# Performance work log

Measured on AMD Instinct MI355X. Metric: run time of the kernel, lower is better.

Reference implementation:

```python
import jax, jax.numpy as jnp
import numpy as np

N_G, K = 1024, 64
n_G, k = 32, 8          # n_G = sqrt(N_G), k = sqrt(K)
m = n_G * k             # 256
M = N_G * K             # 65536

def _mask_indices(k):
    # concentric square rings of a k x k grid; ring 0 = outermost
    ii, jj = np.meshgrid(np.arange(k), np.arange(k), indexing='ij')
    d = np.minimum(np.minimum(ii, jj), np.minimum(k - 1 - ii, k - 1 - jj))
    rings = [(d == r) for r in range((k + 1) // 2)]
    groups = np.array_split(np.arange(len(rings)), 3)  # outer / inter / inner ring groups
    merged = [np.any(np.stack([rings[i] for i in g]), axis=0) for g in groups]
    outer, inter, inner = merged
    flat = lambda msk: np.nonzero(msk.ravel())[0]
    return flat(inner), flat(inter), flat(outer)

IDX_INNER, IDX_INTER, IDX_OUTER = _mask_indices(k)  # sizes 4, 12, 48

def setup_inputs() -> dict:
    key = jax.random.key(0)
    ks = jax.random.split(key, 13)
    p = lambda kk, sh: 0.05 * jax.random.normal(kk, sh, dtype=jnp.float32)
    return {
        'pgi': jax.random.normal(ks[0], (32, M, 3), dtype=jnp.float32),
        'W_lift': p(ks[1], (3, 32)),   'b_lift': p(ks[2], (32,)),
        'W_code': p(ks[3], (96, 128)), 'b_code': p(ks[4], (128,)),
        'W_h1': p(ks[5], (128, 64)),   'b_h1': p(ks[6], (64,)),
        'W_h2': p(ks[7], (64, 32)),    'b_h2': p(ks[8], (32,)),
        'W_h3': p(ks[9], (32, 16)),    'b_h3': p(ks[10], (16,)),
        'W_h4': p(ks[11], (16, 3)),    'b_h4': jnp.zeros((3,), jnp.float32),
    }

def _lift_max(pts, W, b):
    # pts: [B, N_G, n_sel, 3] -> SMLP(3->32, leakyrelu 0.2) -> max over points
    h = jax.nn.leaky_relu(jnp.einsum('bgpc,cd->bgpd', pts, W) + b, 0.2)
    return h.max(axis=2)  # [B, N_G, 32]

def reference(pgi, W_lift, b_lift, W_code, b_code, W_h1, b_h1, W_h2, b_h2, W_h3, b_h3, W_h4, b_h4):
    B = pgi.shape[0]
    # pgi [B, M, 3] is a row-major m x m grid; partition into N_G blocks of k x k points
    grid = pgi.reshape(B, n_G, k, n_G, k, 3)
    blocks = grid.transpose(0, 1, 3, 2, 4, 5).reshape(B, N_G, K, 3)
    v_inner = _lift_max(blocks[:, :, IDX_INNER], W_lift, b_lift)
    v_inter = _lift_max(blocks[:, :, IDX_INTER], W_lift, b_lift)
    v_outer = _lift_max(blocks[:, :, IDX_OUTER], W_lift, b_lift)
    v = jnp.concatenate([v_inner, v_inter, v_outer], axis=-1)   # [B, N_G, 96]
    v_code = jax.nn.leaky_relu(v @ W_code + b_code, 0.2)        # [B, N_G, 128]
    h = jax.nn.relu(v_code @ W_h1 + b_h1)
    h = jax.nn.relu(h @ W_h2 + b_h2)
    h = jax.nn.relu(h @ W_h3 + b_h3)
    return h @ W_h4 + b_h4                                      # guidance_pts [B, N_G, 3]
```

## Files before the change

kernel.cpp:

```cpp
#include <hip/hip_runtime.h>
#include <math.h>


typedef _Float16 h8  __attribute__((ext_vector_type(8)));
typedef _Float16 h2t __attribute__((ext_vector_type(2)));
typedef float    f4  __attribute__((ext_vector_type(4)));

constexpr int SVH = 104;
constexpr int SWC = 104;
constexpr int SCH = 136;
constexpr int S1H = 72;
constexpr int S2H = 40;
constexpr int S3H = 24;

constexpr int OFF_V = 0;
constexpr int OFF_W = 13312;
constexpr int OFF_C = 39936;
constexpr int W1T_O = 0;
constexpr int W2T_O = 8704;
constexpr int W3T_O = 11008;

__global__ __launch_bounds__(256, 2)
void flatnet_fused(const float* __restrict__ pgi,
                   const float* __restrict__ Wl, const float* __restrict__ bl,
                   const float* __restrict__ Wc, const float* __restrict__ bc,
                   const float* __restrict__ W1, const float* __restrict__ b1,
                   const float* __restrict__ W2, const float* __restrict__ b2,
                   const float* __restrict__ W3, const float* __restrict__ b3,
                   const float* __restrict__ W4, const float* __restrict__ b4,
                   float* __restrict__ out)
{
    __shared__ __align__(16) char lds[57344];
    _Float16* sV = (_Float16*)(lds + OFF_V);
    _Float16* sW = (_Float16*)(lds + OFF_W);
    _Float16* sC = (_Float16*)(lds + OFF_C);

    const int t    = threadIdx.x;
    const int blk  = blockIdx.x;
    const int lane = t & 63;
    const int wv   = t >> 6;
    const int l15  = lane & 15;
    const int lq   = lane >> 4;

    {
        const int ln = t >> 2;
        const int q  = t & 3;
        const int gn = blk * 64 + ln;
        const int b  = gn >> 10;
        const int g  = gn & 1023;
        const int gi = g >> 5, gj = g & 31;

        float w0[8], w1[8], w2[8], bb[8];
        #pragma unroll
        for (int d = 0; d < 8; ++d) {
            const int dd = q * 8 + d;
            w0[d] = Wl[dd];
            w1[d] = Wl[32 + dd];
            w2[d] = Wl[64 + dd];
            bb[d] = bl[dd];
        }

        float gm[3][8];
        #pragma unroll
        for (int gg = 0; gg < 3; ++gg)
            #pragma unroll
            for (int d = 0; d < 8; ++d) gm[gg][d] = -INFINITY;

        constexpr int GT[8][8] = {
            {2,2,2,2,2,2,2,2},
            {2,2,2,2,2,2,2,2},
            {2,2,1,1,1,1,2,2},
            {2,2,1,0,0,1,2,2},
            {2,2,1,0,0,1,2,2},
            {2,2,1,1,1,1,2,2},
            {2,2,2,2,2,2,2,2},
            {2,2,2,2,2,2,2,2},
        };

        const size_t rowbase = (size_t)b * 65536 + ((size_t)gi * 8) * 256 + (size_t)gj * 8;
        #pragma unroll
        for (int pi = 0; pi < 8; ++pi) {
            const float4* src = (const float4*)(pgi + (rowbase + (size_t)pi * 256) * 3);
            float f[24];
            #pragma unroll
            for (int l = 0; l < 6; ++l) {
                const float4 v = src[l];
                f[l*4+0] = v.x; f[l*4+1] = v.y; f[l*4+2] = v.z; f[l*4+3] = v.w;
            }
            #pragma unroll
            for (int pj = 0; pj < 8; ++pj) {
                const int grp = GT[pi][pj];
                const float x = f[pj*3], y = f[pj*3+1], z = f[pj*3+2];
                #pragma unroll
                for (int d = 0; d < 8; ++d) {
                    float v = fmaf(x, w0[d], bb[d]);
                    v = fmaf(y, w1[d], v);
                    v = fmaf(z, w2[d], v);
                    gm[grp][d] = fmaxf(gm[grp][d], v);
                }
            }
        }
        #pragma unroll
        for (int gg = 0; gg < 3; ++gg) {
            h8 hv;
            #pragma unroll
            for (int d = 0; d < 8; ++d) {
                const float v = gm[gg][d];
                hv[d] = (_Float16)fmaxf(v, 0.2f * v);
            }
            *(h8*)&sV[ln*SVH + gg*32 + q*8] = hv;
        }

        #pragma unroll
        for (int i = 0; i < 6; ++i) {
            const int u = t + (i << 8);
            const int k = (u >> 5) << 1;
            const int n = (u & 31) << 2;
            const float4 r0 = *(const float4*)&Wc[k*128 + n];
            const float4 r1 = *(const float4*)&Wc[(k+1)*128 + n];
            h2t p0 = {(_Float16)r0.x, (_Float16)r1.x};
            h2t p1 = {(_Float16)r0.y, (_Float16)r1.y};
            h2t p2 = {(_Float16)r0.z, (_Float16)r1.z};
            h2t p3 = {(_Float16)r0.w, (_Float16)r1.w};
            *(h2t*)&sW[(n+0)*SWC + k] = p0;
            *(h2t*)&sW[(n+1)*SWC + k] = p1;
            *(h2t*)&sW[(n+2)*SWC + k] = p2;
            *(h2t*)&sW[(n+3)*SWC + k] = p3;
        }
    }
    __syncthreads();

    {
        const int nt0 = wv * 2;
        h8 Bf[2][3];
        float bcv[2];
        #pragma unroll
        for (int nn = 0; nn < 2; ++nn) {
            bcv[nn] = bc[(nt0+nn)*16 + l15];
            #pragma unroll
            for (int kq = 0; kq < 3; ++kq)
                Bf[nn][kq] = *(const h8*)&sW[((nt0+nn)*16 + l15)*SWC + kq*32 + lq*8];
        }
        f4 acc[4][2];
        #pragma unroll
        for (int mt = 0; mt < 4; ++mt)
            #pragma unroll
            for (int nn = 0; nn < 2; ++nn) {
                f4 z = {bcv[nn], bcv[nn], bcv[nn], bcv[nn]};
                acc[mt][nn] = z;
            }
        #pragma unroll
        for (int mt = 0; mt < 4; ++mt) {
            h8 Af[3];
            #pragma unroll
            for (int kq = 0; kq < 3; ++kq)
                Af[kq] = *(const h8*)&sV[(mt*16 + l15)*SVH + kq*32 + lq*8];
            #pragma unroll
            for (int kq = 0; kq < 3; ++kq) {
                acc[mt][0] = __builtin_amdgcn_mfma_f32_16x16x32_f16(Af[kq], Bf[0][kq], acc[mt][0], 0, 0, 0);
                acc[mt][1] = __builtin_amdgcn_mfma_f32_16x16x32_f16(Af[kq], Bf[1][kq], acc[mt][1], 0, 0, 0);
            }
        }
        __syncthreads();

        #pragma unroll
        for (int mt = 0; mt < 4; ++mt)
            #pragma unroll
            for (int nn = 0; nn < 2; ++nn) {
                const int col = (nt0+nn)*16 + l15;
                #pragma unroll
                for (int r = 0; r < 4; ++r) {
                    const int row = mt*16 + lq*4 + r;
                    const float v = acc[mt][nn][r];
                    sC[row*SCH + col] = (_Float16)fmaxf(v, 0.2f * v);
                }
            }
    }

    {
        #pragma unroll
        for (int i = 0; i < 4; ++i) {
            const int u = t + (i << 8);
            const int k = (u >> 4) << 1;
            const int n = (u & 15) << 2;
            const float4 r0 = *(const float4*)&W1[k*64 + n];
            const float4 r1 = *(const float4*)&W1[(k+1)*64 + n];
            h2t p0 = {(_Float16)r0.x, (_Float16)r1.x};
            h2t p1 = {(_Float16)r0.y, (_Float16)r1.y};
            h2t p2 = {(_Float16)r0.z, (_Float16)r1.z};
            h2t p3 = {(_Float16)r0.w, (_Float16)r1.w};
            *(h2t*)&sW[W1T_O + (n+0)*SCH + k] = p0;
            *(h2t*)&sW[W1T_O + (n+1)*SCH + k] = p1;
            *(h2t*)&sW[W1T_O + (n+2)*SCH + k] = p2;
            *(h2t*)&sW[W1T_O + (n+3)*SCH + k] = p3;
        }
        {
            const int k = (t >> 3) << 1;
            const int n = (t & 7) << 2;
            const float4 r0 = *(const float4*)&W2[k*32 + n];
            const float4 r1 = *(const float4*)&W2[(k+1)*32 + n];
            h2t p0 = {(_Float16)r0.x, (_Float16)r1.x};
            h2t p1 = {(_Float16)r0.y, (_Float16)r1.y};
            h2t p2 = {(_Float16)r0.z, (_Float16)r1.z};
            h2t p3 = {(_Float16)r0.w, (_Float16)r1.w};
            *(h2t*)&sW[W2T_O + (n+0)*S1H + k] = p0;
            *(h2t*)&sW[W2T_O + (n+1)*S1H + k] = p1;
            *(h2t*)&sW[W2T_O + (n+2)*S1H + k] = p2;
            *(h2t*)&sW[W2T_O + (n+3)*S1H + k] = p3;
        }
        if (t < 64) {
            const int k = (t >> 2) << 1;
            const int n = (t & 3) << 2;
            const float4 r0 = *(const float4*)&W3[k*16 + n];
            const float4 r1 = *(const float4*)&W3[(k+1)*16 + n];
            h2t p0 = {(_Float16)r0.x, (_Float16)r1.x};
            h2t p1 = {(_Float16)r0.y, (_Float16)r1.y};
            h2t p2 = {(_Float16)r0.z, (_Float16)r1.z};
            h2t p3 = {(_Float16)r0.w, (_Float16)r1.w};
            *(h2t*)&sW[W3T_O + (n+0)*S2H + k] = p0;
            *(h2t*)&sW[W3T_O + (n+1)*S2H + k] = p1;
            *(h2t*)&sW[W3T_O + (n+2)*S2H + k] = p2;
            *(h2t*)&sW[W3T_O + (n+3)*S2H + k] = p3;
        }
    }
    __syncthreads();

    {
        h8 Bf[4];
        #pragma unroll
        for (int kq = 0; kq < 4; ++kq)
            Bf[kq] = *(const h8*)&sW[W1T_O + (wv*16 + l15)*SCH + kq*32 + lq*8];
        const float bv = b1[wv*16 + l15];
        f4 acc[4];
        #pragma unroll
        for (int mt = 0; mt < 4; ++mt) { f4 z = {bv,bv,bv,bv}; acc[mt] = z; }
        #pragma unroll
        for (int mt = 0; mt < 4; ++mt) {
            #pragma unroll
            for (int kq = 0; kq < 4; ++kq) {
                const h8 Af = *(const h8*)&sC[(mt*16 + l15)*SCH + kq*32 + lq*8];
                acc[mt] = __builtin_amdgcn_mfma_f32_16x16x32_f16(Af, Bf[kq], acc[mt], 0, 0, 0);
            }
        }
        __syncthreads();
        #pragma unroll
        for (int mt = 0; mt < 4; ++mt) {
            const int col = wv*16 + l15;
            #pragma unroll
            for (int r = 0; r < 4; ++r) {
                const int row = mt*16 + lq*4 + r;
                sV[row*S1H + col] = (_Float16)fmaxf(acc[mt][r], 0.f);
            }
        }
    }
    __syncthreads();

    {
        const int nt  = wv & 1;
        const int mt0 = (wv >> 1) << 1;
        h8 Bf[2];
        #pragma unroll
        for (int kq = 0; kq < 2; ++kq)
            Bf[kq] = *(const h8*)&sW[W2T_O + (nt*16 + l15)*S1H + kq*32 + lq*8];
        const float bv = b2[nt*16 + l15];
        f4 acc[2];
        #pragma unroll
        for (int mi = 0; mi < 2; ++mi) { f4 z = {bv,bv,bv,bv}; acc[mi] = z; }
        #pragma unroll
        for (int mi = 0; mi < 2; ++mi) {
            #pragma unroll
            for (int kq = 0; kq < 2; ++kq) {
                const h8 Af = *(const h8*)&sV[((mt0+mi)*16 + l15)*S1H + kq*32 + lq*8];
                acc[mi] = __builtin_amdgcn_mfma_f32_16x16x32_f16(Af, Bf[kq], acc[mi], 0, 0, 0);
            }
        }
        __syncthreads();
        #pragma unroll
        for (int mi = 0; mi < 2; ++mi) {
            const int col = nt*16 + l15;
            #pragma unroll
            for (int r = 0; r < 4; ++r) {
                const int row = (mt0+mi)*16 + lq*4 + r;
                sC[row*S2H + col] = (_Float16)fmaxf(acc[mi][r], 0.f);
            }
        }
    }
    __syncthreads();

    {
        const h8 Bf = *(const h8*)&sW[W3T_O + l15*S2H + lq*8];
        const float bv = b3[l15];
        f4 acc = {bv,bv,bv,bv};
        const h8 Af = *(const h8*)&sC[(wv*16 + l15)*S2H + lq*8];
        acc = __builtin_amdgcn_mfma_f32_16x16x32_f16(Af, Bf, acc, 0, 0, 0);
        #pragma unroll
        for (int r = 0; r < 4; ++r) {
            const int row = wv*16 + lq*4 + r;
            sC[2560 + row*S3H + l15] = (_Float16)fmaxf(acc[r], 0.f);
        }
    }
    __syncthreads();

    if (t < 64) {
        const h8 h0 = *(const h8*)&sC[2560 + t*S3H];
        const h8 h1 = *(const h8*)&sC[2560 + t*S3H + 8];
        float a[16];
        #pragma unroll
        for (int j = 0; j < 8; ++j) { a[j] = (float)h0[j]; a[8+j] = (float)h1[j]; }
        float acc0 = b4[0], acc1 = b4[1], acc2 = b4[2];
        #pragma unroll
        for (int j = 0; j < 16; ++j) {
            acc0 = fmaf(a[j], W4[j*3+0], acc0);
            acc1 = fmaf(a[j], W4[j*3+1], acc1);
            acc2 = fmaf(a[j], W4[j*3+2], acc2);
        }
        const size_t gn = (size_t)blk * 64 + t;
        out[gn*3 + 0] = acc0;
        out[gn*3 + 1] = acc1;
        out[gn*3 + 2] = acc2;
    }
}

extern "C" void kernel_launch(void* const* d_in, const int* in_sizes, int n_in,
                              void* d_out, int out_size, void* d_ws, size_t ws_size,
                              hipStream_t stream)
{
    const float* pgi = (const float*)d_in[0];
    const float* Wl  = (const float*)d_in[1];
    const float* bl  = (const float*)d_in[2];
    const float* Wc  = (const float*)d_in[3];
    const float* bc  = (const float*)d_in[4];
    const float* W1  = (const float*)d_in[5];
    const float* b1  = (const float*)d_in[6];
    const float* W2  = (const float*)d_in[7];
    const float* b2  = (const float*)d_in[8];
    const float* W3  = (const float*)d_in[9];
    const float* b3  = (const float*)d_in[10];
    const float* W4  = (const float*)d_in[11];
    const float* b4  = (const float*)d_in[12];

    hipLaunchKernelGGL(flatnet_fused, dim3(512), dim3(256), 0, stream,
                       pgi, Wl, bl, Wc, bc, W1, b1, W2, b2, W3, b3, W4, b4,
                       (float*)d_out);
}
```

Measured before the change: 101.0 us.

## Pre-convert weights in separate kernel, halve groups per block, split rows across threads

```diff
diff --git a/kernel.cpp b/kernel.cpp
--- a/kernel.cpp
+++ b/kernel.cpp
@@ -2,38 +2,56 @@
 #include <math.h>
 
 
-typedef _Float16 h8  __attribute__((ext_vector_type(8)));
-typedef _Float16 h2t __attribute__((ext_vector_type(2)));
-typedef float    f4  __attribute__((ext_vector_type(4)));
+typedef _Float16 h8 __attribute__((ext_vector_type(8)));
+typedef float    f4 __attribute__((ext_vector_type(4)));
+
+constexpr int WCT_O = 0;
+constexpr int W1T_O = 12288;
+constexpr int W2T_O = 20480;
+constexpr int W3T_O = 22528;
+constexpr int WS_N  = 23040;
 
 constexpr int SVH = 104;
-constexpr int SWC = 104;
 constexpr int SCH = 136;
 constexpr int S1H = 72;
 constexpr int S2H = 40;
 constexpr int S3H = 24;
-
-constexpr int OFF_V = 0;
-constexpr int OFF_W = 13312;
-constexpr int OFF_C = 39936;
-constexpr int W1T_O = 0;
-constexpr int W2T_O = 8704;
-constexpr int W3T_O = 11008;
-
-__global__ __launch_bounds__(256, 2)
+constexpr int H3O = 32 * S2H;
+
+__global__ __launch_bounds__(256)
+void cvt_weights(const float* __restrict__ Wc, const float* __restrict__ W1,
+                 const float* __restrict__ W2, const float* __restrict__ W3,
+                 _Float16* __restrict__ ws16)
+{
+    const int i = blockIdx.x * 256 + threadIdx.x;
+    float v;
+    if (i < 12288) {
+        const int n = i / 96, k = i - n * 96;
+        v = Wc[k * 128 + n];
+    } else if (i < 20480) {
+        const int j = i - 12288, n = j >> 7, k = j & 127;
+        v = W1[k * 64 + n];
+    } else if (i < 22528) {
+        const int j = i - 20480, n = j >> 6, k = j & 63;
+        v = W2[k * 32 + n];
+    } else {
+        const int j = i - 22528, n = j >> 5, k = j & 31;
+        v = W3[k * 16 + n];
+    }
+    ws16[i] = (_Float16)v;
+}
+
+__global__ __launch_bounds__(256, 4)
 void flatnet_fused(const float* __restrict__ pgi,
                    const float* __restrict__ Wl, const float* __restrict__ bl,
-                   const float* __restrict__ Wc, const float* __restrict__ bc,
-                   const float* __restrict__ W1, const float* __restrict__ b1,
-                   const float* __restrict__ W2, const float* __restrict__ b2,
-                   const float* __restrict__ W3, const float* __restrict__ b3,
+                   const _Float16* __restrict__ ws16,
+                   const float* __restrict__ bc, const float* __restrict__ b1,
+                   const float* __restrict__ b2, const float* __restrict__ b3,
                    const float* __restrict__ W4, const float* __restrict__ b4,
                    float* __restrict__ out)
 {
-    __shared__ __align__(16) char lds[57344];
-    _Float16* sV = (_Float16*)(lds + OFF_V);
-    _Float16* sW = (_Float16*)(lds + OFF_W);
-    _Float16* sC = (_Float16*)(lds + OFF_C);
+    __shared__ __align__(16) _Float16 sV[32 * SVH];
+    __shared__ __align__(16) _Float16 sC[32 * SCH];
 
     const int t    = threadIdx.x;
     const int blk  = blockIdx.x;
@@ -43,9 +61,11 @@
     const int lq   = lane >> 4;
 
     {
-        const int ln = t >> 2;
-        const int q  = t & 3;
-        const int gn = blk * 64 + ln;
+        const int ln = t >> 3;
+        const int q  = t & 7;
+        const int dq = (q & 3) * 8;
+        const int h  = q >> 2;
+        const int gn = blk * 32 + ln;
         const int b  = gn >> 10;
         const int g  = gn & 1023;
         const int gi = g >> 5, gj = g & 31;
@@ -53,11 +73,10 @@
         float w0[8], w1[8], w2[8], bb[8];
         #pragma unroll
         for (int d = 0; d < 8; ++d) {
-            const int dd = q * 8 + d;
-            w0[d] = Wl[dd];
-            w1[d] = Wl[32 + dd];
-            w2[d] = Wl[64 + dd];
-            bb[d] = bl[dd];
+            w0[d] = Wl[dq + d];
+            w1[d] = Wl[32 + dq + d];
+            w2[d] = Wl[64 + dq + d];
+            bb[d] = bl[dq + d];
         }
 
         float gm[3][8];
@@ -66,21 +85,18 @@
             #pragma unroll
             for (int d = 0; d < 8; ++d) gm[gg][d] = -INFINITY;
 
-        constexpr int GT[8][8] = {
+        constexpr int GT4[4][8] = {
             {2,2,2,2,2,2,2,2},
             {2,2,2,2,2,2,2,2},
             {2,2,1,1,1,1,2,2},
             {2,2,1,0,0,1,2,2},
-            {2,2,1,0,0,1,2,2},
-            {2,2,1,1,1,1,2,2},
-            {2,2,2,2,2,2,2,2},
-            {2,2,2,2,2,2,2,2},
         };
 
         const size_t rowbase = (size_t)b * 65536 + ((size_t)gi * 8) * 256 + (size_t)gj * 8;
         #pragma unroll
-        for (int pi = 0; pi < 8; ++pi) {
-            const float4* src = (const float4*)(pgi + (rowbase + (size_t)pi * 256) * 3);
+        for (int pi = 0; pi < 4; ++pi) {
+            const int prow = h ? (7 - pi) : pi;
+            const float4* src = (const float4*)(pgi + (rowbase + (size_t)prow * 256) * 3);
             float f[24];
             #pragma unroll
             for (int l = 0; l < 6; ++l) {
@@ -89,7 +105,7 @@
             }
             #pragma unroll
             for (int pj = 0; pj < 8; ++pj) {
-                const int grp = GT[pi][pj];
+                const int grp = GT4[pi][pj];
                 const float x = f[pj*3], y = f[pj*3+1], z = f[pj*3+2];
                 #pragma unroll
                 for (int d = 0; d < 8; ++d) {
@@ -101,31 +117,22 @@
             }
         }
         #pragma unroll
-        for (int gg = 0; gg < 3; ++gg) {
-            h8 hv;
-            #pragma unroll
-            for (int d = 0; d < 8; ++d) {
-                const float v = gm[gg][d];
-                hv[d] = (_Float16)fmaxf(v, 0.2f * v);
-            }
-            *(h8*)&sV[ln*SVH + gg*32 + q*8] = hv;
-        }
-
-        #pragma unroll
-        for (int i = 0; i < 6; ++i) {
-            const int u = t + (i << 8);
-            const int k = (u >> 5) << 1;
-            const int n = (u & 31) << 2;
-            const float4 r0 = *(const float4*)&Wc[k*128 + n];
-            const float4 r1 = *(const float4*)&Wc[(k+1)*128 + n];
-            h2t p0 = {(_Float16)r0.x, (_Float16)r1.x};
-            h2t p1 = {(_Float16)r0.y, (_Float16)r1.y};
-            h2t p2 = {(_Float16)r0.z, (_Float16)r1.z};
-            h2t p3 = {(_Float16)r0.w, (_Float16)r1.w};
-            *(h2t*)&sW[(n+0)*SWC + k] = p0;
-            *(h2t*)&sW[(n+1)*SWC + k] = p1;
-            *(h2t*)&sW[(n+2)*SWC + k] = p2;
-            *(h2t*)&sW[(n+3)*SWC + k] = p3;
+        for (int gg = 0; gg < 3; ++gg)
+            #pragma unroll
+            for (int d = 0; d < 8; ++d)
+                gm[gg][d] = fmaxf(gm[gg][d], __shfl_xor(gm[gg][d], 4));
+
+        if (h == 0) {
+            #pragma unroll
+            for (int gg = 0; gg < 3; ++gg) {
+                h8 hv;
+                #pragma unroll
+                for (int d = 0; d < 8; ++d) {
+                    const float v = gm[gg][d];
+                    hv[d] = (_Float16)fmaxf(v, 0.2f * v);
+                }
+                *(h8*)&sV[ln*SVH + gg*32 + dq] = hv;
+            }
         }
     }
     __syncthreads();
@@ -139,32 +146,28 @@
             bcv[nn] = bc[(nt0+nn)*16 + l15];
             #pragma unroll
             for (int kq = 0; kq < 3; ++kq)
-                Bf[nn][kq] = *(const h8*)&sW[((nt0+nn)*16 + l15)*SWC + kq*32 + lq*8];
-        }
-        f4 acc[4][2];
-        #pragma unroll
-        for (int mt = 0; mt < 4; ++mt)
+                Bf[nn][kq] = *(const h8*)&ws16[WCT_O + ((nt0+nn)*16 + l15)*96 + kq*32 + lq*8];
+        }
+        f4 acc[2][2];
+        #pragma unroll
+        for (int mt = 0; mt < 2; ++mt)
             #pragma unroll
             for (int nn = 0; nn < 2; ++nn) {
                 f4 z = {bcv[nn], bcv[nn], bcv[nn], bcv[nn]};
                 acc[mt][nn] = z;
             }
         #pragma unroll
-        for (int mt = 0; mt < 4; ++mt) {
-            h8 Af[3];
-            #pragma unroll
-            for (int kq = 0; kq < 3; ++kq)
-                Af[kq] = *(const h8*)&sV[(mt*16 + l15)*SVH + kq*32 + lq*8];
+        for (int mt = 0; mt < 2; ++mt) {
             #pragma unroll
             for (int kq = 0; kq < 3; ++kq) {
-                acc[mt][0] = __builtin_amdgcn_mfma_f32_16x16x32_f16(Af[kq], Bf[0][kq], acc[mt][0], 0, 0, 0);
-                acc[mt][1] = __builtin_amdgcn_mfma_f32_16x16x32_f16(Af[kq], Bf[1][kq], acc[mt][1], 0, 0, 0);
+                const h8 Af = *(const h8*)&sV[(mt*16 + l15)*SVH + kq*32 + lq*8];
+                acc[mt][0] = __builtin_amdgcn_mfma_f32_16x16x32_f16(Af, Bf[0][kq], acc[mt][0], 0, 0, 0);
+                acc[mt][1] = __builtin_amdgcn_mfma_f32_16x16x32_f16(Af, Bf[1][kq], acc[mt][1], 0, 0, 0);
             }
         }
         __syncthreads();
-
-        #pragma unroll
-        for (int mt = 0; mt < 4; ++mt)
+        #pragma unroll
+        for (int mt = 0; mt < 2; ++mt)
             #pragma unroll
             for (int nn = 0; nn < 2; ++nn) {
                 const int col = (nt0+nn)*16 + l15;
@@ -176,75 +179,27 @@
                 }
             }
     }
-
-    {
-        #pragma unroll
-        for (int i = 0; i < 4; ++i) {
-            const int u = t + (i << 8);
-            const int k = (u >> 4) << 1;
-            const int n = (u & 15) << 2;
-            const float4 r0 = *(const float4*)&W1[k*64 + n];
-            const float4 r1 = *(const float4*)&W1[(k+1)*64 + n];
-            h2t p0 = {(_Float16)r0.x, (_Float16)r1.x};
-            h2t p1 = {(_Float16)r0.y, (_Float16)r1.y};
-            h2t p2 = {(_Float16)r0.z, (_Float16)r1.z};
-            h2t p3 = {(_Float16)r0.w, (_Float16)r1.w};
-            *(h2t*)&sW[W1T_O + (n+0)*SCH + k] = p0;
-            *(h2t*)&sW[W1T_O + (n+1)*SCH + k] = p1;
-            *(h2t*)&sW[W1T_O + (n+2)*SCH + k] = p2;
-            *(h2t*)&sW[W1T_O + (n+3)*SCH + k] = p3;
-        }
-        {
-            const int k = (t >> 3) << 1;
-            const int n = (t & 7) << 2;
-            const float4 r0 = *(const float4*)&W2[k*32 + n];
-            const float4 r1 = *(const float4*)&W2[(k+1)*32 + n];
-            h2t p0 = {(_Float16)r0.x, (_Float16)r1.x};
-            h2t p1 = {(_Float16)r0.y, (_Float16)r1.y};
-            h2t p2 = {(_Float16)r0.z, (_Float16)r1.z};
-            h2t p3 = {(_Float16)r0.w, (_Float16)r1.w};
-            *(h2t*)&sW[W2T_O + (n+0)*S1H + k] = p0;
-            *(h2t*)&sW[W2T_O + (n+1)*S1H + k] = p1;
-            *(h2t*)&sW[W2T_O + (n+2)*S1H + k] = p2;
-            *(h2t*)&sW[W2T_O + (n+3)*S1H + k] = p3;
-        }
-        if (t < 64) {
-            const int k = (t >> 2) << 1;
-            const int n = (t & 3) << 2;
-            const float4 r0 = *(const float4*)&W3[k*16 + n];
-            const float4 r1 = *(const float4*)&W3[(k+1)*16 + n];
-            h2t p0 = {(_Float16)r0.x, (_Float16)r1.x};
-            h2t p1 = {(_Float16)r0.y, (_Float16)r1.y};
-            h2t p2 = {(_Float16)r0.z, (_Float16)r1.z};
-            h2t p3 = {(_Float16)r0.w, (_Float16)r1.w};
-            *(h2t*)&sW[W3T_O + (n+0)*S2H + k] = p0;
-            *(h2t*)&sW[W3T_O + (n+1)*S2H + k] = p1;
-            *(h2t*)&sW[W3T_O + (n+2)*S2H + k] = p2;
-            *(h2t*)&sW[W3T_O + (n+3)*S2H + k] = p3;
-        }
-    }
     __syncthreads();
 
     {
         h8 Bf[4];
         #pragma unroll
         for (int kq = 0; kq < 4; ++kq)
-            Bf[kq] = *(const h8*)&sW[W1T_O + (wv*16 + l15)*SCH + kq*32 + lq*8];
+            Bf[kq] = *(const h8*)&ws16[W1T_O + (wv*16 + l15)*128 + kq*32 + lq*8];
         const float bv = b1[wv*16 + l15];
-        f4 acc[4];
-        #pragma unroll
-        for (int mt = 0; mt < 4; ++mt) { f4 z = {bv,bv,bv,bv}; acc[mt] = z; }
-        #pragma unroll
-        for (int mt = 0; mt < 4; ++mt) {
+        f4 acc[2];
+        #pragma unroll
+        for (int mt = 0; mt < 2; ++mt) { f4 z = {bv,bv,bv,bv}; acc[mt] = z; }
+        #pragma unroll
+        for (int mt = 0; mt < 2; ++mt)
             #pragma unroll
             for (int kq = 0; kq < 4; ++kq) {
                 const h8 Af = *(const h8*)&sC[(mt*16 + l15)*SCH + kq*32 + lq*8];
                 acc[mt] = __builtin_amdgcn_mfma_f32_16x16x32_f16(Af, Bf[kq], acc[mt], 0, 0, 0);
             }
-        }
         __syncthreads();
         #pragma unroll
-        for (int mt = 0; mt < 4; ++mt) {
+        for (int mt = 0; mt < 2; ++mt) {
             const int col = wv*16 + l15;
             #pragma unroll
             for (int r = 0; r < 4; ++r) {
@@ -256,54 +211,46 @@
     __syncthreads();
 
     {
-        const int nt  = wv & 1;
-        const int mt0 = (wv >> 1) << 1;
+        const int mt = wv & 1;
+        const int nt = wv >> 1;
         h8 Bf[2];
         #pragma unroll
         for (int kq = 0; kq < 2; ++kq)
-            Bf[kq] = *(const h8*)&sW[W2T_O + (nt*16 + l15)*S1H + kq*32 + lq*8];
+            Bf[kq] = *(const h8*)&ws16[W2T_O + (nt*16 + l15)*64 + kq*32 + lq*8];
         const float bv = b2[nt*16 + l15];
-        f4 acc[2];
-        #pragma unroll
-        for (int mi = 0; mi < 2; ++mi) { f4 z = {bv,bv,bv,bv}; acc[mi] = z; }
-        #pragma unroll
-        for (int mi = 0; mi < 2; ++mi) {
-            #pragma unroll
-            for (int kq = 0; kq < 2; ++kq) {
-                const h8 Af = *(const h8*)&sV[((mt0+mi)*16 + l15)*S1H + kq*32 + lq*8];
-                acc[mi] = __builtin_amdgcn_mfma_f32_16x16x32_f16(Af, Bf[kq], acc[mi], 0, 0, 0);
-            }
+        f4 acc = {bv, bv, bv, bv};
+        #pragma unroll
+        for (int kq = 0; kq < 2; ++kq) {
+            const h8 Af = *(const h8*)&sV[(mt*16 + l15)*S1H + kq*32 + lq*8];
+            acc = __builtin_amdgcn_mfma_f32_16x16x32_f16(Af, Bf[kq], acc, 0, 0, 0);
         }
         __syncthreads();
-        #pragma unroll
-        for (int mi = 0; mi < 2; ++mi) {
-            const int col = nt*16 + l15;
-            #pragma unroll
-            for (int r = 0; r < 4; ++r) {
-                const int row = (mt0+mi)*16 + lq*4 + r;
-                sC[row*S2H + col] = (_Float16)fmaxf(acc[mi][r], 0.f);
-            }
-        }
-    }
-    __syncthreads();
-
-    {
-        const h8 Bf = *(const h8*)&sW[W3T_O + l15*S2H + lq*8];
+        const int col = nt*16 + l15;
+        #pragma unroll
+        for (int r = 0; r < 4; ++r) {
+            const int row = mt*16 + lq*4 + r;
+            sC[row*S2H + col] = (_Float16)fmaxf(acc[r], 0.f);
+        }
+    }
+    __syncthreads();
+
+    if (wv < 2) {
+        const h8 Bf = *(const h8*)&ws16[W3T_O + l15*32 + lq*8];
         const float bv = b3[l15];
-        f4 acc = {bv,bv,bv,bv};
+        f4 acc = {bv, bv, bv, bv};
         const h8 Af = *(const h8*)&sC[(wv*16 + l15)*S2H + lq*8];
         acc = __builtin_amdgcn_mfma_f32_16x16x32_f16(Af, Bf, acc, 0, 0, 0);
         #pragma unroll
         for (int r = 0; r < 4; ++r) {
             const int row = wv*16 + lq*4 + r;
-            sC[2560 + row*S3H + l15] = (_Float16)fmaxf(acc[r], 0.f);
-        }
-    }
-    __syncthreads();
-
-    if (t < 64) {
-        const h8 h0 = *(const h8*)&sC[2560 + t*S3H];
-        const h8 h1 = *(const h8*)&sC[2560 + t*S3H + 8];
+            sC[H3O + row*S3H + l15] = (_Float16)fmaxf(acc[r], 0.f);
+        }
+    }
+    __syncthreads();
+
+    if (t < 32) {
+        const h8 h0 = *(const h8*)&sC[H3O + t*S3H];
+        const h8 h1 = *(const h8*)&sC[H3O + t*S3H + 8];
         float a[16];
         #pragma unroll
         for (int j = 0; j < 8; ++j) { a[j] = (float)h0[j]; a[8+j] = (float)h1[j]; }
@@ -314,7 +261,7 @@
             acc1 = fmaf(a[j], W4[j*3+1], acc1);
             acc2 = fmaf(a[j], W4[j*3+2], acc2);
         }
-        const size_t gn = (size_t)blk * 64 + t;
+        const size_t gn = (size_t)blk * 32 + t;
         out[gn*3 + 0] = acc0;
         out[gn*3 + 1] = acc1;
         out[gn*3 + 2] = acc2;
@@ -339,7 +286,11 @@
     const float* W4  = (const float*)d_in[11];
     const float* b4  = (const float*)d_in[12];
 
-    hipLaunchKernelGGL(flatnet_fused, dim3(512), dim3(256), 0, stream,
-                       pgi, Wl, bl, Wc, bc, W1, b1, W2, b2, W3, b3, W4, b4,
+    _Float16* ws16 = (_Float16*)d_ws;
+
+    hipLaunchKernelGGL(cvt_weights, dim3(90), dim3(256), 0, stream,
+                       Wc, W1, W2, W3, ws16);
+    hipLaunchKernelGGL(flatnet_fused, dim3(1024), dim3(256), 0, stream,
+                       pgi, Wl, bl, ws16, bc, b1, b2, b3, W4, b4,
                        (float*)d_out);
 }
```

New measurement: 102.0 us. Within noise of the previous version (+1.1%).
